# Kernel optimization log

Hardware: AMD Instinct MI355X
Metric: run time of the kernel (lower is better)

The kernel has to match this reference:

```python
import jax, jax.numpy as jnp
import numpy as np

N, E, HDIM, EDIM, MSG_H, UPD_H = 50000, 640000, 128, 32, 128, 128
LN_EPS = 1e-5


def setup_inputs() -> dict:
    key = jax.random.key(0)
    ks = jax.random.split(key, 12)
    def lin(k, fan_in, fan_out):
        return jax.random.normal(k, (fan_in, fan_out), dtype=jnp.float32) / np.sqrt(fan_in)
    h = jax.random.normal(ks[0], (N, HDIM), dtype=jnp.float32)
    edge_index = jax.random.randint(ks[1], (2, E), 0, N, dtype=jnp.int32)
    edge_attr = jax.random.normal(ks[2], (E, EDIM), dtype=jnp.float32)
    return {
        "h": h,
        "edge_index": edge_index,
        "edge_attr": edge_attr,
        # edge MLP: Linear(2*hdim+edim -> msg_hidden), ReLU, Linear(msg_hidden -> hdim)
        "ew1": lin(ks[3], 2 * HDIM + EDIM, MSG_H),
        "eb1": jnp.zeros((MSG_H,), jnp.float32),
        "ew2": lin(ks[4], MSG_H, HDIM),
        "eb2": jnp.zeros((HDIM,), jnp.float32),
        # node MLP: Linear(2*hdim -> upd_hidden), ReLU, Linear(upd_hidden -> hdim)
        "nw1": lin(ks[5], 2 * HDIM, UPD_H),
        "nb1": jnp.zeros((UPD_H,), jnp.float32),
        "nw2": lin(ks[6], UPD_H, HDIM),
        "nb2": jnp.zeros((HDIM,), jnp.float32),
        # LayerNorm(hdim)
        "gamma": jnp.ones((HDIM,), jnp.float32),
        "beta": jnp.zeros((HDIM,), jnp.float32),
    }


def reference(h, edge_index, edge_attr, ew1, eb1, ew2, eb2, nw1, nb1, nw2, nb2, gamma, beta):
    src, dst = edge_index[0], edge_index[1]
    # gather + concat -> edge MLP  (eval mode: dropout inactive, edge_dropout off)
    m_in = jnp.concatenate([h[src], h[dst], edge_attr], axis=1)       # [E, 2H+EDIM]
    m = jax.nn.relu(m_in @ ew1 + eb1) @ ew2 + eb2                     # [E, H]
    # scatter-add messages into destination nodes
    agg = jax.ops.segment_sum(m, dst, num_segments=h.shape[0])        # [N, H]
    # node update MLP
    u_in = jnp.concatenate([h, agg], axis=1)                          # [N, 2H]
    h_upd = jax.nn.relu(u_in @ nw1 + nb1) @ nw2 + nb2                 # [N, H]
    # residual + LayerNorm
    x = h + h_upd
    mu = jnp.mean(x, axis=-1, keepdims=True)
    var = jnp.mean(jnp.square(x - mu), axis=-1, keepdims=True)
    return (x - mu) * jax.lax.rsqrt(var + LN_EPS) * gamma + beta
```

## Files before the change

### kernel.cpp

```cpp
#include <hip/hip_runtime.h>
#include <cstdint>

#define HD 128
#define ED 32
#define BME 64
#define BMN 128
#define PAD_E 296
#define PAD_N 264
#define PAD_T 136

typedef _Float16 f16;
typedef __attribute__((ext_vector_type(2))) _Float16 f16x2;
typedef __attribute__((ext_vector_type(4))) _Float16 f16x4;
typedef __attribute__((ext_vector_type(8))) _Float16 f16x8;
typedef __attribute__((ext_vector_type(4))) float    f32x4;

__device__ __forceinline__ f32x4 mfma16(f16x8 a, f16x8 b, f32x4 c) {
    return __builtin_amdgcn_mfma_f32_16x16x32_f16(a, b, c, 0, 0, 0);
}
__device__ __forceinline__ f16x8 cvt8(const float* p) {
    const float4 a0 = *(const float4*)p;
    const float4 a1 = *(const float4*)(p + 4);
    f16x8 v;
    v[0] = (f16)a0.x; v[1] = (f16)a0.y; v[2] = (f16)a0.z; v[3] = (f16)a0.w;
    v[4] = (f16)a1.x; v[5] = (f16)a1.y; v[6] = (f16)a1.z; v[7] = (f16)a1.w;
    return v;
}

__global__ __launch_bounds__(256) void zero_f32(float4* p, long n4) {
    long i = (long)blockIdx.x * blockDim.x + threadIdx.x;
    const long stride = (long)gridDim.x * blockDim.x;
    const float4 z = make_float4(0.f, 0.f, 0.f, 0.f);
    for (; i < n4; i += stride) p[i] = z;
}
__global__ __launch_bounds__(256) void zero_i32(int* p, int n) {
    int i = blockIdx.x * blockDim.x + threadIdx.x;
    if (i < n) p[i] = 0;
}
__global__ __launch_bounds__(256)
void cvt_f16_kernel(const float* __restrict__ x, f16* __restrict__ y, long n8) {
    long i = blockIdx.x * 256 + threadIdx.x;
    const long stride = (long)gridDim.x * 256;
    for (; i < n8; i += stride) *(f16x8*)(y + i * 8) = cvt8(x + i * 8);
}
__global__ __launch_bounds__(256)
void pack_w_kernel(const float* __restrict__ w, f16* __restrict__ wp, int KT) {
    const int idx = blockIdx.x * 256 + threadIdx.x;
    if (idx >= KT * 8 * 64) return;
    const int l  = idx & 63;
    const int fr = idx >> 6;
    const int ht = fr & 1, wv = (fr >> 1) & 3, kt = fr >> 3;
    const int li = l & 15, q = l >> 4;
    const float* p = w + (size_t)(32 * kt + 8 * q) * HD + 32 * wv + 16 * ht + li;
    f16x8 v;
#pragma unroll
    for (int e2 = 0; e2 < 8; ++e2) v[e2] = (f16)p[(size_t)e2 * HD];
    *(f16x8*)(wp + (size_t)idx * 8) = v;
}

__global__ __launch_bounds__(256)
void hist_kernel(const int* __restrict__ eidx, int* __restrict__ rank,
                 int* __restrict__ cnt, int E) {
    int e = blockIdx.x * 256 + threadIdx.x;
    if (e < E) rank[e] = atomicAdd(&cnt[eidx[E + e]], 1);
}
__global__ __launch_bounds__(1024)
void scan_kernel(const int* __restrict__ cnt, int* __restrict__ rs, int N) {
    __shared__ int wsum[16];
    __shared__ int s_carry;
    const int t = threadIdx.x, lane = t & 63, wid = t >> 6;
    if (t == 0) s_carry = 0;
    __syncthreads();
    for (int base = 0; base < N; base += 1024) {
        const int i = base + t;
        const int v = (i < N) ? cnt[i] : 0;
        int incl = v;
#pragma unroll
        for (int off = 1; off < 64; off <<= 1) {
            int u = __shfl_up(incl, off, 64);
            if (lane >= off) incl += u;
        }
        if (lane == 63) wsum[wid] = incl;
        __syncthreads();
        if (t == 0) {
            int s = 0;
#pragma unroll
            for (int w = 0; w < 16; ++w) { int x = wsum[w]; wsum[w] = s; s += x; }
        }
        __syncthreads();
        const int carry = s_carry;
        if (i < N) rs[i] = carry + wsum[wid] + incl - v;
        __syncthreads();
        if (t == 1023) s_carry = carry + wsum[15] + incl;
        __syncthreads();
    }
    if (threadIdx.x == 0) rs[N] = s_carry;
}
__global__ __launch_bounds__(256)
void pos_kernel(const int* __restrict__ eidx, const int* __restrict__ rs,
                int* __restrict__ pos, int E) {
    int e = blockIdx.x * 256 + threadIdx.x;
    if (e < E) pos[e] = rs[eidx[E + e]] + pos[e];
}

template <int MODE>
__global__ __launch_bounds__(256, 4)
void edge_kernel(const f16*   __restrict__ h16,
                 const int*   __restrict__ eidx,
                 const float* __restrict__ ea,
                 const f16*   __restrict__ w1p,
                 const float* __restrict__ b1,
                 const f16*   __restrict__ w2p,
                 const float* __restrict__ b2,
                 void*        __restrict__ aggm,
                 const int*   __restrict__ pos,
                 int E)
{
    __shared__ __align__(16) f16 sA[BME * PAD_E];
    __shared__ int sIdx[BME];

    const int t  = threadIdx.x;
    const int l  = t & 63;
    const int wv = t >> 6;
    const int li = l & 15;
    const int q  = l >> 4;
    const int ebase = blockIdx.x * BME;

    if (t < BME) {
        const int ec = min(ebase + t, E - 1);
        sIdx[t] = (MODE == 0) ? eidx[E + ec] : pos[ec];
    }

    {
        const int r  = t >> 2;
        const int q4 = t & 3;
        const int ec = min(ebase + r, E - 1);
        const int src = eidx[ec];
        const int dst = eidx[E + ec];
        const f16* hs = h16 + (size_t)src * HD;
        const f16* hd = h16 + (size_t)dst * HD;
        const float* eap = ea + (size_t)ec * ED;
        f16* row = sA + r * PAD_E;
#pragma unroll
        for (int i = 0; i < 9; ++i) {
            const int c = q4 * 72 + i * 8;
            f16x8 v;
            if (c < 2 * HD) v = *(const f16x8*)((c < HD) ? (hs + c) : (hd + c - HD));
            else            v = cvt8(eap + (c - 2 * HD));
            *(f16x8*)(row + c) = v;
        }
    }
    __syncthreads();

    f32x4 acc[2][4];
#pragma unroll
    for (int i = 0; i < 2; ++i)
#pragma unroll
        for (int j = 0; j < 4; ++j) acc[i][j] = (f32x4){0.f, 0.f, 0.f, 0.f};

#pragma unroll 3
    for (int kt = 0; kt < 9; ++kt) {
        const f16x8 a0 = *(const f16x8*)(w1p + ((size_t)(kt * 8 + wv * 2 + 0) * 64 + l) * 8);
        const f16x8 a1 = *(const f16x8*)(w1p + ((size_t)(kt * 8 + wv * 2 + 1) * 64 + l) * 8);
#pragma unroll
        for (int et = 0; et < 4; ++et) {
            const f16x8 b = *(const f16x8*)(sA + (16 * et + li) * PAD_E + 32 * kt + 8 * q);
            acc[0][et] = mfma16(a0, b, acc[0][et]);
            acc[1][et] = mfma16(a1, b, acc[1][et]);
        }
    }
    __syncthreads();

    f16* sT = sA;
#pragma unroll
    for (int ht = 0; ht < 2; ++ht) {
        const int hidb = 32 * wv + 16 * ht + 4 * q;
        const float4 bb = *(const float4*)(b1 + hidb);
#pragma unroll
        for (int et = 0; et < 4; ++et) {
            const f32x4 v = acc[ht][et];
            float x0 = v[0] + bb.x, x1 = v[1] + bb.y,
                  x2 = v[2] + bb.z, x3 = v[3] + bb.w;
            x0 = x0 > 0.f ? x0 : 0.f;  x1 = x1 > 0.f ? x1 : 0.f;
            x2 = x2 > 0.f ? x2 : 0.f;  x3 = x3 > 0.f ? x3 : 0.f;
            f16x4 o; o[0] = (f16)x0; o[1] = (f16)x1; o[2] = (f16)x2; o[3] = (f16)x3;
            *(f16x4*)(sT + (16 * et + li) * PAD_T + hidb) = o;
        }
    }
    __syncthreads();

    f32x4 acc2[2][4];
#pragma unroll
    for (int i = 0; i < 2; ++i)
#pragma unroll
        for (int j = 0; j < 4; ++j) acc2[i][j] = (f32x4){0.f, 0.f, 0.f, 0.f};

#pragma unroll
    for (int kt = 0; kt < 4; ++kt) {
        const f16x8 a0 = *(const f16x8*)(w2p + ((size_t)(kt * 8 + wv * 2 + 0) * 64 + l) * 8);
        const f16x8 a1 = *(const f16x8*)(w2p + ((size_t)(kt * 8 + wv * 2 + 1) * 64 + l) * 8);
#pragma unroll
        for (int et = 0; et < 4; ++et) {
            const f16x8 b = *(const f16x8*)(sT + (16 * et + li) * PAD_T + 32 * kt + 8 * q);
            acc2[0][et] = mfma16(a0, b, acc2[0][et]);
            acc2[1][et] = mfma16(a1, b, acc2[1][et]);
        }
    }

    if (MODE == 0) {
        float* agg = (float*)aggm;
#pragma unroll
        for (int ht = 0; ht < 2; ++ht) {
            const int hidb = 32 * wv + 16 * ht + 4 * q;
            const float4 bb = *(const float4*)(b2 + hidb);
#pragma unroll
            for (int et = 0; et < 4; ++et) {
                const int edge = 16 * et + li;
                if (ebase + edge < E) {
                    float* p = agg + (size_t)sIdx[edge] * HD + hidb;
                    const f32x4 v = acc2[ht][et];
                    atomicAdd(p + 0, v[0] + bb.x);
                    atomicAdd(p + 1, v[1] + bb.y);
                    atomicAdd(p + 2, v[2] + bb.z);
                    atomicAdd(p + 3, v[3] + bb.w);
                }
            }
        }
    } else {
        __syncthreads();
#pragma unroll
        for (int ht = 0; ht < 2; ++ht) {
            const int hidb = 32 * wv + 16 * ht + 4 * q;
            const float4 bb = *(const float4*)(b2 + hidb);
#pragma unroll
            for (int et = 0; et < 4; ++et) {
                const f32x4 v = acc2[ht][et];
                f16x4 o;
                o[0] = (f16)(v[0] + bb.x); o[1] = (f16)(v[1] + bb.y);
                o[2] = (f16)(v[2] + bb.z); o[3] = (f16)(v[3] + bb.w);
                *(f16x4*)(sT + (16 * et + li) * PAD_T + hidb) = o;
            }
        }
        __syncthreads();
        f16* m = (f16*)aggm;
#pragma unroll
        for (int i = 0; i < 4; ++i) {
            const int idx = t + i * 256;
            const int row = idx >> 4;
            const int c8  = (idx & 15) * 8;
            if (ebase + row < E) {
                const f16x8 v = *(const f16x8*)(sT + row * PAD_T + c8);
                *(f16x8*)(m + (size_t)sIdx[row] * HD + c8) = v;
            }
        }
    }
}

__global__ __launch_bounds__(256)
void gather_kernel(const f16* __restrict__ m, const int* __restrict__ rs,
                   f16* __restrict__ aggb, int N)
{
    const int n = blockIdx.x * 4 + (threadIdx.x >> 6);
    if (n >= N) return;
    const int lane = threadIdx.x & 63;
    const int s = rs[n], e = rs[n + 1];
    const f16* base = m + (size_t)s * HD + lane * 2;
    const int cnt = e - s;
    float a0 = 0.f, b0 = 0.f, a1 = 0.f, b1 = 0.f;
    int j = 0;
    for (; j + 2 <= cnt; j += 2) {
        const f16x2 u = *(const f16x2*)(base + (size_t)j * HD);
        const f16x2 v = *(const f16x2*)(base + (size_t)(j + 1) * HD);
        a0 += (float)u[0]; b0 += (float)u[1];
        a1 += (float)v[0]; b1 += (float)v[1];
    }
    if (j < cnt) {
        const f16x2 u = *(const f16x2*)(base + (size_t)j * HD);
        a0 += (float)u[0]; b0 += (float)u[1];
    }
    f16x2 r; r[0] = (f16)(a0 + a1); r[1] = (f16)(b0 + b1);
    *(f16x2*)(aggb + (size_t)n * HD + lane * 2) = r;
}

template <int CSR>
__global__ __launch_bounds__(256, 2)
void node_kernel(const f16*   __restrict__ h16,
                 const float* __restrict__ h,
                 const f16*   __restrict__ aggb,
                 const float* __restrict__ aggf,
                 const f16*   __restrict__ w1p,
                 const float* __restrict__ b1,
                 const f16*   __restrict__ w2p,
                 const float* __restrict__ b2,
                 const float* __restrict__ gamma,
                 const float* __restrict__ beta,
                 float*       __restrict__ out,
                 int N)
{
    __shared__ __align__(16) f16 sA[BMN * PAD_N];
    __shared__ f16   sT[BMN * PAD_T];
    __shared__ float sMV[2 * BMN];

    const int t  = threadIdx.x;
    const int l  = t & 63;
    const int wv = t >> 6;
    const int li = l & 15;
    const int q  = l >> 4;
    const int nbase = blockIdx.x * BMN;

    {
        const int r = t >> 1, half = t & 1;
        const int node = min(nbase + r, N - 1);
        f16* rowp = sA + r * PAD_N + half * HD;
        if (half == 0) {
            const f16* src = h16 + (size_t)node * HD;
#pragma unroll
            for (int i = 0; i < 16; ++i)
                *(f16x8*)(rowp + i * 8) = *(const f16x8*)(src + i * 8);
        } else if (CSR) {
            const f16* src = aggb + (size_t)node * HD;
#pragma unroll
            for (int i = 0; i < 16; ++i)
                *(f16x8*)(rowp + i * 8) = *(const f16x8*)(src + i * 8);
        } else {
            const float* src = aggf + (size_t)node * HD;
#pragma unroll
            for (int i = 0; i < 16; ++i)
                *(f16x8*)(rowp + i * 8) = cvt8(src + i * 8);
        }
    }
    __syncthreads();

    f32x4 acc[2][8];
#pragma unroll
    for (int i = 0; i < 2; ++i)
#pragma unroll
        for (int j = 0; j < 8; ++j) acc[i][j] = (f32x4){0.f, 0.f, 0.f, 0.f};

#pragma unroll 2
    for (int kt = 0; kt < 8; ++kt) {
        const f16x8 a0 = *(const f16x8*)(w1p + ((size_t)(kt * 8 + wv * 2 + 0) * 64 + l) * 8);
        const f16x8 a1 = *(const f16x8*)(w1p + ((size_t)(kt * 8 + wv * 2 + 1) * 64 + l) * 8);
#pragma unroll
        for (int et = 0; et < 8; ++et) {
            const f16x8 b = *(const f16x8*)(sA + (16 * et + li) * PAD_N + 32 * kt + 8 * q);
            acc[0][et] = mfma16(a0, b, acc[0][et]);
            acc[1][et] = mfma16(a1, b, acc[1][et]);
        }
    }
    __syncthreads();

#pragma unroll
    for (int ht = 0; ht < 2; ++ht) {
        const int hidb = 32 * wv + 16 * ht + 4 * q;
        const float4 bb = *(const float4*)(b1 + hidb);
#pragma unroll
        for (int et = 0; et < 8; ++et) {
            const f32x4 v = acc[ht][et];
            float x0 = v[0] + bb.x, x1 = v[1] + bb.y,
                  x2 = v[2] + bb.z, x3 = v[3] + bb.w;
            x0 = x0 > 0.f ? x0 : 0.f;  x1 = x1 > 0.f ? x1 : 0.f;
            x2 = x2 > 0.f ? x2 : 0.f;  x3 = x3 > 0.f ? x3 : 0.f;
            f16x4 o; o[0] = (f16)x0; o[1] = (f16)x1; o[2] = (f16)x2; o[3] = (f16)x3;
            *(f16x4*)(sT + (16 * et + li) * PAD_T + hidb) = o;
        }
    }
    __syncthreads();

    f32x4 acc2[2][8];
#pragma unroll
    for (int i = 0; i < 2; ++i)
#pragma unroll
        for (int j = 0; j < 8; ++j) acc2[i][j] = (f32x4){0.f, 0.f, 0.f, 0.f};

#pragma unroll
    for (int kt = 0; kt < 4; ++kt) {
        const f16x8 a0 = *(const f16x8*)(w2p + ((size_t)(kt * 8 + wv * 2 + 0) * 64 + l) * 8);
        const f16x8 a1 = *(const f16x8*)(w2p + ((size_t)(kt * 8 + wv * 2 + 1) * 64 + l) * 8);
#pragma unroll
        for (int et = 0; et < 8; ++et) {
            const f16x8 b = *(const f16x8*)(sT + (16 * et + li) * PAD_T + 32 * kt + 8 * q);
            acc2[0][et] = mfma16(a0, b, acc2[0][et]);
            acc2[1][et] = mfma16(a1, b, acc2[1][et]);
        }
    }
    __syncthreads();

    float* sX = (float*)sA;
#pragma unroll
    for (int ht = 0; ht < 2; ++ht) {
        const int hidb = 32 * wv + 16 * ht + 4 * q;
        const float4 bb = *(const float4*)(b2 + hidb);
#pragma unroll
        for (int et = 0; et < 8; ++et) {
            const int node = 16 * et + li;
            const int nc   = min(nbase + node, N - 1);
            const float4 hv = *(const float4*)(h + (size_t)nc * HD + hidb);
            const f32x4 v = acc2[ht][et];
            f32x4 x;
            x[0] = v[0] + bb.x + hv.x;
            x[1] = v[1] + bb.y + hv.y;
            x[2] = v[2] + bb.z + hv.z;
            x[3] = v[3] + bb.w + hv.w;
            *(f32x4*)(sX + (size_t)node * 132 + hidb) = x;
        }
    }
    __syncthreads();

    {
        const int node  = t >> 1;
        const int half2 = t & 1;
        const float* px = sX + node * 132 + half2 * 64;
        float s = 0.f, sq = 0.f;
#pragma unroll
        for (int i = 0; i < 16; ++i) {
            const float4 v = *(const float4*)(px + i * 4);
            s  += v.x + v.y + v.z + v.w;
            sq += v.x * v.x + v.y * v.y + v.z * v.z + v.w * v.w;
        }
        s  += __shfl_xor(s, 1);
        sq += __shfl_xor(sq, 1);
        if (!half2) {
            const float mean = s * (1.f / HD);
            const float var  = sq * (1.f / HD) - mean * mean;
            sMV[node]       = mean;
            sMV[BMN + node] = rsqrtf(var + 1e-5f);
        }
    }
    __syncthreads();

#pragma unroll
    for (int i = 0; i < 16; ++i) {
        const int idx  = t + i * 256;
        const int node = idx >> 5;
        const int c4   = (idx & 31) * 4;
        if (nbase + node < N) {
            const float4 xv = *(const float4*)(sX + node * 132 + c4);
            const float4 g4 = *(const float4*)(gamma + c4);
            const float4 b4 = *(const float4*)(beta + c4);
            const float mean = sMV[node];
            const float rstd = sMV[BMN + node];
            float4 o;
            o.x = (xv.x - mean) * rstd * g4.x + b4.x;
            o.y = (xv.y - mean) * rstd * g4.y + b4.y;
            o.z = (xv.z - mean) * rstd * g4.z + b4.z;
            o.w = (xv.w - mean) * rstd * g4.w + b4.w;
            *(float4*)(out + (size_t)(nbase + node) * HD + c4) = o;
        }
    }
}

extern "C" void kernel_launch(void* const* d_in, const int* in_sizes, int n_in,
                              void* d_out, int out_size, void* d_ws, size_t ws_size,
                              hipStream_t stream)
{
    const float* h     = (const float*)d_in[0];
    const int*   eidx  = (const int*)  d_in[1];
    const float* ea    = (const float*)d_in[2];
    const float* ew1   = (const float*)d_in[3];
    const float* eb1   = (const float*)d_in[4];
    const float* ew2   = (const float*)d_in[5];
    const float* eb2   = (const float*)d_in[6];
    const float* nw1   = (const float*)d_in[7];
    const float* nb1   = (const float*)d_in[8];
    const float* nw2   = (const float*)d_in[9];
    const float* nb2   = (const float*)d_in[10];
    const float* gamma = (const float*)d_in[11];
    const float* beta  = (const float*)d_in[12];
    float* out = (float*)d_out;

    const int N = in_sizes[0] / HD;
    const int E = in_sizes[1] / 2;

    size_t off = 0;
    auto alloc = [&](size_t bytes) {
        size_t o = off; off += (bytes + 255) & ~(size_t)255; return o;
    };
    const size_t o_m    = alloc((size_t)E * HD * sizeof(f16));
    const size_t o_agb  = alloc((size_t)N * HD * sizeof(f16));
    const size_t o_h16  = alloc((size_t)N * HD * sizeof(f16));
    const size_t o_pos  = alloc((size_t)E * sizeof(int));
    const size_t o_rs   = alloc((size_t)(N + 1) * sizeof(int));
    const size_t o_cnt  = alloc((size_t)N * sizeof(int));
    const size_t o_w1p  = alloc((size_t)9 * 8 * 64 * 8 * sizeof(f16));
    const size_t o_w2p  = alloc((size_t)4 * 8 * 64 * 8 * sizeof(f16));
    const size_t o_n1p  = alloc((size_t)8 * 8 * 64 * 8 * sizeof(f16));
    const size_t o_n2p  = alloc((size_t)4 * 8 * 64 * 8 * sizeof(f16));
    const bool csr = (off <= ws_size);
    char* ws = (char*)d_ws;

    if (csr) {
        f16* mb   = (f16*)(ws + o_m);
        f16* aggb = (f16*)(ws + o_agb);
        f16* h16  = (f16*)(ws + o_h16);
        int* pos  = (int*)(ws + o_pos);
        int* rs   = (int*)(ws + o_rs);
        int* cnt  = (int*)(ws + o_cnt);
        f16* w1p  = (f16*)(ws + o_w1p);
        f16* w2p  = (f16*)(ws + o_w2p);
        f16* n1p  = (f16*)(ws + o_n1p);
        f16* n2p  = (f16*)(ws + o_n2p);

        zero_i32<<<(N + 255) / 256, 256, 0, stream>>>(cnt, N);
        hist_kernel<<<(E + 255) / 256, 256, 0, stream>>>(eidx, pos, cnt, E);
        scan_kernel<<<1, 1024, 0, stream>>>(cnt, rs, N);
        pos_kernel<<<(E + 255) / 256, 256, 0, stream>>>(eidx, rs, pos, E);
        cvt_f16_kernel<<<2048, 256, 0, stream>>>(h, h16, (long)N * HD / 8);
        pack_w_kernel<<<18, 256, 0, stream>>>(ew1, w1p, 9);
        pack_w_kernel<<<8,  256, 0, stream>>>(ew2, w2p, 4);
        pack_w_kernel<<<16, 256, 0, stream>>>(nw1, n1p, 8);
        pack_w_kernel<<<8,  256, 0, stream>>>(nw2, n2p, 4);
        edge_kernel<1><<<(E + BME - 1) / BME, 256, 0, stream>>>(
            h16, eidx, ea, w1p, eb1, w2p, eb2, (void*)mb, pos, E);
        gather_kernel<<<(N + 3) / 4, 256, 0, stream>>>(mb, rs, aggb, N);
        node_kernel<1><<<(N + BMN - 1) / BMN, 256, 0, stream>>>(
            h16, h, aggb, nullptr, n1p, nb1, n2p, nb2, gamma, beta, out, N);
    } else {
        size_t foff = 0;
        auto falloc = [&](size_t bytes) {
            size_t o = foff; foff += (bytes + 255) & ~(size_t)255; return o;
        };
        float* agg = (float*)(ws + falloc((size_t)N * HD * sizeof(float)));
        f16*   h16 = (f16*)  (ws + falloc((size_t)N * HD * sizeof(f16)));
        f16*   w1p = (f16*)  (ws + falloc((size_t)9 * 8 * 64 * 8 * sizeof(f16)));
        f16*   w2p = (f16*)  (ws + falloc((size_t)4 * 8 * 64 * 8 * sizeof(f16)));
        f16*   n1p = (f16*)  (ws + falloc((size_t)8 * 8 * 64 * 8 * sizeof(f16)));
        f16*   n2p = (f16*)  (ws + falloc((size_t)4 * 8 * 64 * 8 * sizeof(f16)));

        zero_f32<<<1024, 256, 0, stream>>>((float4*)agg, (long)N * HD / 4);
        cvt_f16_kernel<<<2048, 256, 0, stream>>>(h, h16, (long)N * HD / 8);
        pack_w_kernel<<<18, 256, 0, stream>>>(ew1, w1p, 9);
        pack_w_kernel<<<8,  256, 0, stream>>>(ew2, w2p, 4);
        pack_w_kernel<<<16, 256, 0, stream>>>(nw1, n1p, 8);
        pack_w_kernel<<<8,  256, 0, stream>>>(nw2, n2p, 4);
        edge_kernel<0><<<(E + BME - 1) / BME, 256, 0, stream>>>(
            h16, eidx, ea, w1p, eb1, w2p, eb2, (void*)agg, nullptr, E);
        node_kernel<0><<<(N + BMN - 1) / BMN, 256, 0, stream>>>(
            h16, h, nullptr, agg, n1p, nb1, n2p, nb2, gamma, beta, out, N);
    }
}
```

Measured before the change: 327.0 us.

## Make edge kernel persistent with register-resident weights and prefetched gathers

The edge kernel becomes a persistent grid-stride loop over 64-edge tiles. Each thread keeps the packed W1/W2 fragments in registers for the whole loop, and the gather of the next tile's source/destination/edge rows is prefetched into registers while the current tile's MFMAs run. The node kernel also hoists its weight fragments into registers and reuses sA for the intermediate tile, and the four weight-pack launches are merged into one. In exchange, register pressure rises (launch bounds drop to 2 blocks per CU), which may lower occupancy and reduce latency hiding.

```diff
diff --git a/kernel.cpp b/kernel.cpp
--- a/kernel.cpp
+++ b/kernel.cpp
@@ -8,6 +8,7 @@
 #define PAD_E 296
 #define PAD_N 264
 #define PAD_T 136
+#define EGRID 512
 
 typedef _Float16 f16;
 typedef __attribute__((ext_vector_type(2))) _Float16 f16x2;
@@ -44,14 +45,23 @@
     for (; i < n8; i += stride) *(f16x8*)(y + i * 8) = cvt8(x + i * 8);
 }
 __global__ __launch_bounds__(256)
-void pack_w_kernel(const float* __restrict__ w, f16* __restrict__ wp, int KT) {
-    const int idx = blockIdx.x * 256 + threadIdx.x;
-    if (idx >= KT * 8 * 64) return;
+void pack_all_kernel(const float* __restrict__ ew1, const float* __restrict__ ew2,
+                     const float* __restrict__ nw1, const float* __restrict__ nw2,
+                     f16* __restrict__ w1p, f16* __restrict__ w2p,
+                     f16* __restrict__ n1p, f16* __restrict__ n2p)
+{
+    const int b = blockIdx.x;
+    const float* w; f16* wp; int base;
+    if (b < 18)      { w = ew1; wp = w1p; base = b; }
+    else if (b < 26) { w = ew2; wp = w2p; base = b - 18; }
+    else if (b < 42) { w = nw1; wp = n1p; base = b - 26; }
+    else             { w = nw2; wp = n2p; base = b - 42; }
+    const int idx = base * 256 + threadIdx.x;
     const int l  = idx & 63;
     const int fr = idx >> 6;
-    const int ht = fr & 1, wv = (fr >> 1) & 3, kt = fr >> 3;
-    const int li = l & 15, q = l >> 4;
-    const float* p = w + (size_t)(32 * kt + 8 * q) * HD + 32 * wv + 16 * ht + li;
+    const int ht = fr & 1, wvv = (fr >> 1) & 3, kt = fr >> 3;
+    const int lii = l & 15, qq = l >> 4;
+    const float* p = w + (size_t)(32 * kt + 8 * qq) * HD + 32 * wvv + 16 * ht + lii;
     f16x8 v;
 #pragma unroll
     for (int e2 = 0; e2 < 8; ++e2) v[e2] = (f16)p[(size_t)e2 * HD];
@@ -104,7 +114,7 @@
 }
 
 template <int MODE>
-__global__ __launch_bounds__(256, 4)
+__global__ __launch_bounds__(256, 2)
 void edge_kernel(const f16*   __restrict__ h16,
                  const int*   __restrict__ eidx,
                  const float* __restrict__ ea,
@@ -114,143 +124,157 @@
                  const float* __restrict__ b2,
                  void*        __restrict__ aggm,
                  const int*   __restrict__ pos,
-                 int E)
+                 int E, int ntiles)
 {
     __shared__ __align__(16) f16 sA[BME * PAD_E];
-    __shared__ int sIdx[BME];
+    __shared__ __align__(16) f16 sT[BME * PAD_T];
+    __shared__ int sIdx[2][BME];
 
     const int t  = threadIdx.x;
     const int l  = t & 63;
     const int wv = t >> 6;
     const int li = l & 15;
     const int q  = l >> 4;
-    const int ebase = blockIdx.x * BME;
-
-    if (t < BME) {
-        const int ec = min(ebase + t, E - 1);
-        sIdx[t] = (MODE == 0) ? eidx[E + ec] : pos[ec];
-    }
-
-    {
-        const int r  = t >> 2;
-        const int q4 = t & 3;
-        const int ec = min(ebase + r, E - 1);
+    const int r  = t >> 2;
+    const int q4 = t & 3;
+
+    f16x8 A1[2][9], A2[2][4];
+#pragma unroll
+    for (int ht = 0; ht < 2; ++ht) {
+#pragma unroll
+        for (int kt = 0; kt < 9; ++kt)
+            A1[ht][kt] = *(const f16x8*)(w1p + ((size_t)(kt * 8 + wv * 2 + ht) * 64 + l) * 8);
+#pragma unroll
+        for (int kt = 0; kt < 4; ++kt)
+            A2[ht][kt] = *(const f16x8*)(w2p + ((size_t)(kt * 8 + wv * 2 + ht) * 64 + l) * 8);
+    }
+
+    f16x8 d[9];
+    int   psr = 0;
+    auto prefetch = [&](int tile) {
+        const int ec  = min(tile * BME + r, E - 1);
         const int src = eidx[ec];
         const int dst = eidx[E + ec];
+        psr = (MODE == 0) ? dst : pos[ec];
         const f16* hs = h16 + (size_t)src * HD;
         const f16* hd = h16 + (size_t)dst * HD;
         const float* eap = ea + (size_t)ec * ED;
-        f16* row = sA + r * PAD_E;
 #pragma unroll
         for (int i = 0; i < 9; ++i) {
             const int c = q4 * 72 + i * 8;
-            f16x8 v;
-            if (c < 2 * HD) v = *(const f16x8*)((c < HD) ? (hs + c) : (hd + c - HD));
-            else            v = cvt8(eap + (c - 2 * HD));
-            *(f16x8*)(row + c) = v;
-        }
-    }
-    __syncthreads();
-
-    f32x4 acc[2][4];
-#pragma unroll
-    for (int i = 0; i < 2; ++i)
-#pragma unroll
-        for (int j = 0; j < 4; ++j) acc[i][j] = (f32x4){0.f, 0.f, 0.f, 0.f};
-
-#pragma unroll 3
-    for (int kt = 0; kt < 9; ++kt) {
-        const f16x8 a0 = *(const f16x8*)(w1p + ((size_t)(kt * 8 + wv * 2 + 0) * 64 + l) * 8);
-        const f16x8 a1 = *(const f16x8*)(w1p + ((size_t)(kt * 8 + wv * 2 + 1) * 64 + l) * 8);
-#pragma unroll
-        for (int et = 0; et < 4; ++et) {
-            const f16x8 b = *(const f16x8*)(sA + (16 * et + li) * PAD_E + 32 * kt + 8 * q);
-            acc[0][et] = mfma16(a0, b, acc[0][et]);
-            acc[1][et] = mfma16(a1, b, acc[1][et]);
-        }
-    }
-    __syncthreads();
-
-    f16* sT = sA;
-#pragma unroll
-    for (int ht = 0; ht < 2; ++ht) {
-        const int hidb = 32 * wv + 16 * ht + 4 * q;
-        const float4 bb = *(const float4*)(b1 + hidb);
-#pragma unroll
-        for (int et = 0; et < 4; ++et) {
-            const f32x4 v = acc[ht][et];
-            float x0 = v[0] + bb.x, x1 = v[1] + bb.y,
-                  x2 = v[2] + bb.z, x3 = v[3] + bb.w;
-            x0 = x0 > 0.f ? x0 : 0.f;  x1 = x1 > 0.f ? x1 : 0.f;
-            x2 = x2 > 0.f ? x2 : 0.f;  x3 = x3 > 0.f ? x3 : 0.f;
-            f16x4 o; o[0] = (f16)x0; o[1] = (f16)x1; o[2] = (f16)x2; o[3] = (f16)x3;
-            *(f16x4*)(sT + (16 * et + li) * PAD_T + hidb) = o;
-        }
-    }
-    __syncthreads();
-
-    f32x4 acc2[2][4];
-#pragma unroll
-    for (int i = 0; i < 2; ++i)
-#pragma unroll
-        for (int j = 0; j < 4; ++j) acc2[i][j] = (f32x4){0.f, 0.f, 0.f, 0.f};
-
-#pragma unroll
-    for (int kt = 0; kt < 4; ++kt) {
-        const f16x8 a0 = *(const f16x8*)(w2p + ((size_t)(kt * 8 + wv * 2 + 0) * 64 + l) * 8);
-        const f16x8 a1 = *(const f16x8*)(w2p + ((size_t)(kt * 8 + wv * 2 + 1) * 64 + l) * 8);
-#pragma unroll
-        for (int et = 0; et < 4; ++et) {
-            const f16x8 b = *(const f16x8*)(sT + (16 * et + li) * PAD_T + 32 * kt + 8 * q);
-            acc2[0][et] = mfma16(a0, b, acc2[0][et]);
-            acc2[1][et] = mfma16(a1, b, acc2[1][et]);
-        }
-    }
-
-    if (MODE == 0) {
-        float* agg = (float*)aggm;
+            d[i] = (c < HD)     ? *(const f16x8*)(hs + c)
+                 : (c < 2 * HD) ? *(const f16x8*)(hd + c - HD)
+                                : cvt8(eap + (c - 2 * HD));
+        }
+    };
+
+    int tb = blockIdx.x;
+    if (tb < ntiles) prefetch(tb);
+    int par = 0;
+
+    for (; tb < ntiles; tb += gridDim.x, par ^= 1) {
+#pragma unroll
+        for (int i = 0; i < 9; ++i)
+            *(f16x8*)(sA + r * PAD_E + q4 * 72 + i * 8) = d[i];
+        if (q4 == 0) sIdx[par][r] = psr;
+        __syncthreads();
+
+        const int nt = tb + gridDim.x;
+        if (nt < ntiles) prefetch(nt);
+
+        f32x4 acc[2][4];
+#pragma unroll
+        for (int i = 0; i < 2; ++i)
+#pragma unroll
+            for (int j = 0; j < 4; ++j) acc[i][j] = (f32x4){0.f, 0.f, 0.f, 0.f};
+#pragma unroll
+        for (int kt = 0; kt < 9; ++kt) {
+#pragma unroll
+            for (int et = 0; et < 4; ++et) {
+                const f16x8 b = *(const f16x8*)(sA + (16 * et + li) * PAD_E + 32 * kt + 8 * q);
+                acc[0][et] = mfma16(A1[0][kt], b, acc[0][et]);
+                acc[1][et] = mfma16(A1[1][kt], b, acc[1][et]);
+            }
+        }
+
 #pragma unroll
         for (int ht = 0; ht < 2; ++ht) {
             const int hidb = 32 * wv + 16 * ht + 4 * q;
-            const float4 bb = *(const float4*)(b2 + hidb);
+            const float4 bb = *(const float4*)(b1 + hidb);
 #pragma unroll
             for (int et = 0; et < 4; ++et) {
-                const int edge = 16 * et + li;
-                if (ebase + edge < E) {
-                    float* p = agg + (size_t)sIdx[edge] * HD + hidb;
-                    const f32x4 v = acc2[ht][et];
-                    atomicAdd(p + 0, v[0] + bb.x);
-                    atomicAdd(p + 1, v[1] + bb.y);
-                    atomicAdd(p + 2, v[2] + bb.z);
-                    atomicAdd(p + 3, v[3] + bb.w);
+                const f32x4 v = acc[ht][et];
+                float x0 = v[0] + bb.x, x1 = v[1] + bb.y,
+                      x2 = v[2] + bb.z, x3 = v[3] + bb.w;
+                x0 = x0 > 0.f ? x0 : 0.f;  x1 = x1 > 0.f ? x1 : 0.f;
+                x2 = x2 > 0.f ? x2 : 0.f;  x3 = x3 > 0.f ? x3 : 0.f;
+                f16x4 o; o[0] = (f16)x0; o[1] = (f16)x1; o[2] = (f16)x2; o[3] = (f16)x3;
+                *(f16x4*)(sT + (16 * et + li) * PAD_T + hidb) = o;
+            }
+        }
+        __syncthreads();
+
+        f32x4 acc2[2][4];
+#pragma unroll
+        for (int i = 0; i < 2; ++i)
+#pragma unroll
+            for (int j = 0; j < 4; ++j) acc2[i][j] = (f32x4){0.f, 0.f, 0.f, 0.f};
+#pragma unroll
+        for (int kt = 0; kt < 4; ++kt) {
+#pragma unroll
+            for (int et = 0; et < 4; ++et) {
+                const f16x8 b = *(const f16x8*)(sT + (16 * et + li) * PAD_T + 32 * kt + 8 * q);
+                acc2[0][et] = mfma16(A2[0][kt], b, acc2[0][et]);
+                acc2[1][et] = mfma16(A2[1][kt], b, acc2[1][et]);
+            }
+        }
+
+        if (MODE == 0) {
+            float* agg = (float*)aggm;
+#pragma unroll
+            for (int ht = 0; ht < 2; ++ht) {
+                const int hidb = 32 * wv + 16 * ht + 4 * q;
+                const float4 bb = *(const float4*)(b2 + hidb);
+#pragma unroll
+                for (int et = 0; et < 4; ++et) {
+                    const int edge = 16 * et + li;
+                    if (tb * BME + edge < E) {
+                        float* p = agg + (size_t)sIdx[par][edge] * HD + hidb;
+                        const f32x4 v = acc2[ht][et];
+                        atomicAdd(p + 0, v[0] + bb.x);
+                        atomicAdd(p + 1, v[1] + bb.y);
+                        atomicAdd(p + 2, v[2] + bb.z);
+                        atomicAdd(p + 3, v[3] + bb.w);
+                    }
                 }
             }
-        }
-    } else {
-        __syncthreads();
-#pragma unroll
-        for (int ht = 0; ht < 2; ++ht) {
-            const int hidb = 32 * wv + 16 * ht + 4 * q;
-            const float4 bb = *(const float4*)(b2 + hidb);
-#pragma unroll
-            for (int et = 0; et < 4; ++et) {
-                const f32x4 v = acc2[ht][et];
-                f16x4 o;
-                o[0] = (f16)(v[0] + bb.x); o[1] = (f16)(v[1] + bb.y);
-                o[2] = (f16)(v[2] + bb.z); o[3] = (f16)(v[3] + bb.w);
-                *(f16x4*)(sT + (16 * et + li) * PAD_T + hidb) = o;
+            __syncthreads();
+        } else {
+            __syncthreads();
+#pragma unroll
+            for (int ht = 0; ht < 2; ++ht) {
+                const int hidb = 32 * wv + 16 * ht + 4 * q;
+                const float4 bb = *(const float4*)(b2 + hidb);
+#pragma unroll
+                for (int et = 0; et < 4; ++et) {
+                    const f32x4 v = acc2[ht][et];
+                    f16x4 o;
+                    o[0] = (f16)(v[0] + bb.x); o[1] = (f16)(v[1] + bb.y);
+                    o[2] = (f16)(v[2] + bb.z); o[3] = (f16)(v[3] + bb.w);
+                    *(f16x4*)(sT + (16 * et + li) * PAD_T + hidb) = o;
+                }
             }
-        }
-        __syncthreads();
-        f16* m = (f16*)aggm;
-#pragma unroll
-        for (int i = 0; i < 4; ++i) {
-            const int idx = t + i * 256;
-            const int row = idx >> 4;
-            const int c8  = (idx & 15) * 8;
-            if (ebase + row < E) {
-                const f16x8 v = *(const f16x8*)(sT + row * PAD_T + c8);
-                *(f16x8*)(m + (size_t)sIdx[row] * HD + c8) = v;
+            __syncthreads();
+            f16* m = (f16*)aggm;
+#pragma unroll
+            for (int i = 0; i < 4; ++i) {
+                const int idx = t + i * 256;
+                const int row = idx >> 4;
+                const int c8  = (idx & 15) * 8;
+                if (tb * BME + row < E) {
+                    const f16x8 v = *(const f16x8*)(sT + row * PAD_T + c8);
+                    *(f16x8*)(m + (size_t)sIdx[par][row] * HD + c8) = v;
+                }
             }
         }
     }
@@ -278,8 +302,8 @@
         const f16x2 u = *(const f16x2*)(base + (size_t)j * HD);
         a0 += (float)u[0]; b0 += (float)u[1];
     }
-    f16x2 r; r[0] = (f16)(a0 + a1); r[1] = (f16)(b0 + b1);
-    *(f16x2*)(aggb + (size_t)n * HD + lane * 2) = r;
+    f16x2 rr; rr[0] = (f16)(a0 + a1); rr[1] = (f16)(b0 + b1);
+    *(f16x2*)(aggb + (size_t)n * HD + lane * 2) = rr;
 }
 
 template <int CSR>
@@ -298,7 +322,6 @@
                  int N)
 {
     __shared__ __align__(16) f16 sA[BMN * PAD_N];
-    __shared__ f16   sT[BMN * PAD_T];
     __shared__ float sMV[2 * BMN];
 
     const int t  = threadIdx.x;
@@ -329,6 +352,13 @@
                 *(f16x8*)(rowp + i * 8) = cvt8(src + i * 8);
         }
     }
+
+    f16x8 A1[2][8];
+#pragma unroll
+    for (int ht = 0; ht < 2; ++ht)
+#pragma unroll
+        for (int kt = 0; kt < 8; ++kt)
+            A1[ht][kt] = *(const f16x8*)(w1p + ((size_t)(kt * 8 + wv * 2 + ht) * 64 + l) * 8);
     __syncthreads();
 
     f32x4 acc[2][8];
@@ -336,20 +366,25 @@
     for (int i = 0; i < 2; ++i)
 #pragma unroll
         for (int j = 0; j < 8; ++j) acc[i][j] = (f32x4){0.f, 0.f, 0.f, 0.f};
-
-#pragma unroll 2
+#pragma unroll
     for (int kt = 0; kt < 8; ++kt) {
-        const f16x8 a0 = *(const f16x8*)(w1p + ((size_t)(kt * 8 + wv * 2 + 0) * 64 + l) * 8);
-        const f16x8 a1 = *(const f16x8*)(w1p + ((size_t)(kt * 8 + wv * 2 + 1) * 64 + l) * 8);
 #pragma unroll
         for (int et = 0; et < 8; ++et) {
             const f16x8 b = *(const f16x8*)(sA + (16 * et + li) * PAD_N + 32 * kt + 8 * q);
-            acc[0][et] = mfma16(a0, b, acc[0][et]);
-            acc[1][et] = mfma16(a1, b, acc[1][et]);
-        }
-    }
-    __syncthreads();
-
+            acc[0][et] = mfma16(A1[0][kt], b, acc[0][et]);
+            acc[1][et] = mfma16(A1[1][kt], b, acc[1][et]);
+        }
+    }
+    __syncthreads();
+
+    f16x8 A2[2][4];
+#pragma unroll
+    for (int ht = 0; ht < 2; ++ht)
+#pragma unroll
+        for (int kt = 0; kt < 4; ++kt)
+            A2[ht][kt] = *(const f16x8*)(w2p + ((size_t)(kt * 8 + wv * 2 + ht) * 64 + l) * 8);
+
+    f16* sT = sA;
 #pragma unroll
     for (int ht = 0; ht < 2; ++ht) {
         const int hidb = 32 * wv + 16 * ht + 4 * q;
@@ -372,16 +407,13 @@
     for (int i = 0; i < 2; ++i)
 #pragma unroll
         for (int j = 0; j < 8; ++j) acc2[i][j] = (f32x4){0.f, 0.f, 0.f, 0.f};
-
 #pragma unroll
     for (int kt = 0; kt < 4; ++kt) {
-        const f16x8 a0 = *(const f16x8*)(w2p + ((size_t)(kt * 8 + wv * 2 + 0) * 64 + l) * 8);
-        const f16x8 a1 = *(const f16x8*)(w2p + ((size_t)(kt * 8 + wv * 2 + 1) * 64 + l) * 8);
 #pragma unroll
         for (int et = 0; et < 8; ++et) {
             const f16x8 b = *(const f16x8*)(sT + (16 * et + li) * PAD_T + 32 * kt + 8 * q);
-            acc2[0][et] = mfma16(a0, b, acc2[0][et]);
-            acc2[1][et] = mfma16(a1, b, acc2[1][et]);
+            acc2[0][et] = mfma16(A2[0][kt], b, acc2[0][et]);
+            acc2[1][et] = mfma16(A2[1][kt], b, acc2[1][et]);
         }
     }
     __syncthreads();
@@ -471,6 +503,7 @@
 
     const int N = in_sizes[0] / HD;
     const int E = in_sizes[1] / 2;
+    const int ntiles = (E + BME - 1) / BME;
 
     size_t off = 0;
     auto alloc = [&](size_t bytes) {
@@ -506,12 +539,9 @@
         scan_kernel<<<1, 1024, 0, stream>>>(cnt, rs, N);
         pos_kernel<<<(E + 255) / 256, 256, 0, stream>>>(eidx, rs, pos, E);
         cvt_f16_kernel<<<2048, 256, 0, stream>>>(h, h16, (long)N * HD / 8);
-        pack_w_kernel<<<18, 256, 0, stream>>>(ew1, w1p, 9);
-        pack_w_kernel<<<8,  256, 0, stream>>>(ew2, w2p, 4);
-        pack_w_kernel<<<16, 256, 0, stream>>>(nw1, n1p, 8);
-        pack_w_kernel<<<8,  256, 0, stream>>>(nw2, n2p, 4);
-        edge_kernel<1><<<(E + BME - 1) / BME, 256, 0, stream>>>(
-            h16, eidx, ea, w1p, eb1, w2p, eb2, (void*)mb, pos, E);
+        pack_all_kernel<<<50, 256, 0, stream>>>(ew1, ew2, nw1, nw2, w1p, w2p, n1p, n2p);
+        edge_kernel<1><<<EGRID, 256, 0, stream>>>(
+            h16, eidx, ea, w1p, eb1, w2p, eb2, (void*)mb, pos, E, ntiles);
         gather_kernel<<<(N + 3) / 4, 256, 0, stream>>>(mb, rs, aggb, N);
         node_kernel<1><<<(N + BMN - 1) / BMN, 256, 0, stream>>>(
             h16, h, aggb, nullptr, n1p, nb1, n2p, nb2, gamma, beta, out, N);
@@ -529,12 +559,9 @@
 
         zero_f32<<<1024, 256, 0, stream>>>((float4*)agg, (long)N * HD / 4);
         cvt_f16_kernel<<<2048, 256, 0, stream>>>(h, h16, (long)N * HD / 8);
-        pack_w_kernel<<<18, 256, 0, stream>>>(ew1, w1p, 9);
-        pack_w_kernel<<<8,  256, 0, stream>>>(ew2, w2p, 4);
-        pack_w_kernel<<<16, 256, 0, stream>>>(nw1, n1p, 8);
-        pack_w_kernel<<<8,  256, 0, stream>>>(nw2, n2p, 4);
-        edge_kernel<0><<<(E + BME - 1) / BME, 256, 0, stream>>>(
-            h16, eidx, ea, w1p, eb1, w2p, eb2, (void*)agg, nullptr, E);
+        pack_all_kernel<<<50, 256, 0, stream>>>(ew1, ew2, nw1, nw2, w1p, w2p, n1p, n2p);
+        edge_kernel<0><<<EGRID, 256, 0, stream>>>(
+            h16, eidx, ea, w1p, eb1, w2p, eb2, (void*)agg, nullptr, E, ntiles);
         node_kernel<0><<<(N + BMN - 1) / BMN, 256, 0, stream>>>(
             h16, h, nullptr, agg, n1p, nb1, n2p, nb2, gamma, beta, out, N);
     }
```

Result: faster. 298.0 us (-8.9%).
